# Optimization experiments

Measured on AMD Instinct MI355X. Metric: run time of the kernel, lower is better.

Reference implementation:

```python
import jax, jax.numpy as jnp
import numpy as np

B, S, D = 16, 38, 1792          # batch, seq_len, d_model = 768 + 2*512
H, DK = 4, 448                   # heads, head dim (D // H)
NP = 128                         # prototype rows before repeat
TOPK = 3                         # hard-coded in VqaPrototypeModel
INF = 768                        # qamodel.qa_outputs.in_features


def setup_inputs() -> dict:
    key = jax.random.key(0)
    ks = jax.random.split(key, 16)
    sc = lambda d: 1.0 / np.sqrt(d)
    inp = {
        "combined_features": jax.random.normal(ks[0], (B, S, D), jnp.float32),
        "prototype_vectors": jax.random.normal(ks[1], (1, NP, D), jnp.float32),
        "attention_mask": jnp.ones((B, S), jnp.int32),
        # MultiThreadMemory: 4 Linear(d_model, d_model) -> q, k, v, out
        "Wq": jax.random.normal(ks[2], (D, D), jnp.float32) * sc(D),
        "bq": jnp.zeros((D,), jnp.float32),
        "Wk": jax.random.normal(ks[3], (D, D), jnp.float32) * sc(D),
        "bk": jnp.zeros((D,), jnp.float32),
        "Wv": jax.random.normal(ks[4], (D, D), jnp.float32) * sc(D),
        "bv": jnp.zeros((D,), jnp.float32),
        "Wo": jax.random.normal(ks[5], (D, D), jnp.float32) * sc(D),
        "bo": jnp.zeros((D,), jnp.float32),
        # fc: Linear(2*d_model, in_features)
        "Wfc": jax.random.normal(ks[6], (2 * D, INF), jnp.float32) * sc(2 * D),
        "bfc": jnp.zeros((INF,), jnp.float32),
        # stub of qamodel.qa_outputs: Linear(in_features, 2)
        "Wqa": jax.random.normal(ks[7], (INF, 2), jnp.float32) * sc(INF),
        "bqa": jnp.zeros((2,), jnp.float32),
    }
    return inp


def reference(combined_features, prototype_vectors, attention_mask,
              Wq, bq, Wk, bk, Wv, bv, Wo, bo, Wfc, bfc, Wqa, bqa):
    b, s, d = combined_features.shape
    # prototype_vectors.repeat(batch_size, seq_length, 1) -> [B, S*NP, D]
    pv = jnp.tile(prototype_vectors, (b, s, 1))
    m = pv.shape[1]

    q = combined_features @ Wq + bq                     # [B,S,D]
    k = pv @ Wk + bk                                    # [B,M,D]
    v = pv @ Wv + bv                                    # [B,M,D]

    q = q.reshape(b, s, H, DK).transpose(0, 2, 1, 3)    # [B,H,S,DK]
    k = k.reshape(b, m, H, DK).transpose(0, 2, 1, 3)    # [B,H,M,DK]
    v = v.reshape(b, m, H, DK).transpose(0, 2, 1, 3)    # [B,H,M,DK]

    # memory_querying_responding: score + topk + gather + softmax + weighted sum
    scores = jnp.einsum('bhsd,bhmd->bhsm', q, k) / np.sqrt(DK)  # [B,H,S,M]
    sel_scores, idx = jax.lax.top_k(scores, TOPK)               # [B,H,S,TOPK]
    # gather selected prototype values: v[b,h,idx[b,h,s,:],:]
    sel_value = jnp.take_along_axis(v[:, :, None, :, :], idx[..., None], axis=3)
    # sel_value: [B,H,S,TOPK,DK]
    p_attn = jax.nn.softmax(sel_scores.astype(jnp.float32), axis=-1)
    x = jnp.einsum('bhsk,bhskd->bhsd', p_attn, sel_value)       # [B,H,S,DK]
    x = x.transpose(0, 2, 1, 3).reshape(b, s, H * DK)           # [B,S,D]
    response = x @ Wo + bo

    final = jnp.concatenate([combined_features, response], axis=2)  # [B,S,2D]
    reduced = final @ Wfc + bfc                                     # [B,S,INF]
    # qamodel stub: qa_outputs head -> start/end logits stacked on last dim
    logits = reduced @ Wqa + bqa                                    # [B,S,2]
    return logits
```

## Files before the change

### kernel.cpp

```cpp
#include <hip/hip_runtime.h>

#define TM 128
#define TN 128
#define BK 16
#define LDT 132

struct SP {
    const float *p0, *p1, *p2, *p3, *p4, *p5, *p6, *p7;
    float *q0, *q1, *q2;
};

__device__ __forceinline__ float wave_sum(float v) {
    #pragma unroll
    for (int off = 32; off; off >>= 1) v += __shfl_down(v, off);
    return v;
}

__device__ __forceinline__ void colvec2_unit(
    const float* __restrict__ A, int lda, const float* __restrict__ W,
    float* __restrict__ out, int K, int m, int lane)
{
    const float4* a = (const float4*)(A + (long)m * lda);
    float a0 = 0.f, a1 = 0.f;
    for (int i = 0; i < K / 256; ++i) {
        const int d4 = lane + 64 * i;
        float4 xv = a[d4];
        const float4* w = (const float4*)(W + (long)d4 * 8);
        float4 w0 = w[0], w1 = w[1];
        a0 += xv.x*w0.x + xv.y*w0.z + xv.z*w1.x + xv.w*w1.z;
        a1 += xv.x*w0.y + xv.y*w0.w + xv.z*w1.y + xv.w*w1.w;
    }
    a0 = wave_sum(a0); a1 = wave_sum(a1);
    if (lane == 0) { out[m * 2 + 0] = a0; out[m * 2 + 1] = a1; }
}

__device__ __forceinline__ void sbias_unit(
    const float* __restrict__ bq, const float* __restrict__ Kp,
    float* __restrict__ sb, int unit, int lane)
{
    const int h = unit >> 7, p = unit & 127;
    const float* kr = Kp + (long)p * 1792 + h * 448;
    const float* bh = bq + h * 448;
    float s = 0.f;
    #pragma unroll
    for (int i = 0; i < 7; ++i) s = fmaf(bh[lane + 64 * i], kr[lane + 64 * i], s);
    s = wave_sum(s);
    if (lane == 0) sb[unit] = s;
}

__device__ __forceinline__ void wvwoq_unit(
    const float* __restrict__ Wv, const float* __restrict__ WoQ,
    float* __restrict__ out, int d, int h, int lane)
{
    const float* wr = Wv + (long)d * 1792 + h * 448;
    const float* wq = WoQ + h * 448 * 2;
    float s0 = 0.f, s1 = 0.f;
    #pragma unroll
    for (int i = 0; i < 7; ++i) {
        const int j = lane + 64 * i;
        const float v = wr[j];
        s0 = fmaf(v, wq[j * 2 + 0], s0);
        s1 = fmaf(v, wq[j * 2 + 1], s1);
    }
    s0 = wave_sum(s0); s1 = wave_sum(s1);
    if (lane == 0) {
        out[((long)h * 1792 + d) * 2 + 0] = s0;
        out[((long)h * 1792 + d) * 2 + 1] = s1;
    }
}

__device__ __forceinline__ void bias_unit(
    const float* __restrict__ bv, const float* __restrict__ WoQ,
    const float* __restrict__ bfc, const float* __restrict__ Wqa,
    const float* __restrict__ bo, const float* __restrict__ WfbQ,
    const float* __restrict__ bqa,
    float* __restrict__ cv, float* __restrict__ const2, int unit, int lane)
{
    float s0 = 0.f, s1 = 0.f;
    if (unit < 4) {
        const int h = unit;
        #pragma unroll
        for (int i = 0; i < 7; ++i) {
            const int j = h * 448 + lane + 64 * i;
            const float v = bv[j];
            s0 = fmaf(v, WoQ[j * 2 + 0], s0);
            s1 = fmaf(v, WoQ[j * 2 + 1], s1);
        }
    } else {
        for (int k = lane; k < 1792; k += 64) {
            if (k < 768) {
                s0 = fmaf(bfc[k], Wqa[k * 2 + 0], s0);
                s1 = fmaf(bfc[k], Wqa[k * 2 + 1], s1);
            }
            s0 = fmaf(bo[k], WfbQ[k * 2 + 0], s0);
            s1 = fmaf(bo[k], WfbQ[k * 2 + 1], s1);
        }
    }
    s0 = wave_sum(s0); s1 = wave_sum(s1);
    if (lane == 0) {
        if (unit < 4) { cv[unit * 2 + 0] = s0; cv[unit * 2 + 1] = s1; }
        else          { const2[0] = s0 + bqa[0]; const2[1] = s1 + bqa[1]; }
    }
}

template<bool TRANSB, int SIDE>
__global__ __launch_bounds__(512) void gemm_f32(
    const float* __restrict__ A, int lda,
    const float* __restrict__ B, int ldb,
    float* __restrict__ C,
    int M, int N, int K,
    int nsplit, int nbb, int mainZ,
    long sAb, long sBb, SP sp)
{
    const int tid = threadIdx.x;
    if ((int)blockIdx.z >= mainZ) {
        const int bid = ((int)blockIdx.z - mainZ) * (gridDim.x * gridDim.y)
                      + blockIdx.y * gridDim.x + blockIdx.x;
        const int lane = tid & 63;
        const int u = bid * 8 + (tid >> 6);
        if constexpr (SIDE == 1) {
            if (u < 3584) colvec2_unit(sp.p0, 768, sp.p1, sp.q0, 768, u, lane);
        } else if constexpr (SIDE == 2) {
            if (u < 1792)       colvec2_unit(sp.p0, 1792, sp.p1, sp.q0, 1792, u, lane);
            else if (u < 2304)  sbias_unit(sp.p2, sp.p3, sp.q1, u - 1792, lane);
        } else if constexpr (SIDE == 3) {
            if (u < 7168)       wvwoq_unit(sp.p0, sp.p1, sp.q0, u % 1792, u / 1792, lane);
            else if (u < 7173)  bias_unit(sp.p2, sp.p1, sp.p3, sp.p4, sp.p5, sp.p6, sp.p7,
                                          sp.q1, sp.q2, u - 7168, lane);
        }
        return;
    }

    const int kb = blockIdx.z % nsplit;
    const int bb = blockIdx.z / nsplit;
    A += sAb * bb;
    B += sBb * bb;
    const int Kc = K / nsplit;
    const int kbeg = kb * Kc;

    __shared__ float As[2][BK][LDT];
    __shared__ float Bs[2][BK][LDT];

    const int tx = tid & 31, ty = tid >> 5;
    const int rowBase = blockIdx.y * TM;
    const int colBase = blockIdx.x * TN;

    const int ar  = tid >> 2;
    const int akq = (tid & 3) * 4;
    const int bkr = tid >> 5;
    const int bc4 = (tid & 31) * 4;
    const int bn  = tid >> 2;
    const int bkq = (tid & 3) * 4;

    const int row0 = rowBase + ar;
    const bool aok = row0 < M;

    float4 av, bv;
    auto loadA = [&](int k0) {
        av = make_float4(0.f, 0.f, 0.f, 0.f);
        if (aok) av = *(const float4*)&A[(long)row0 * lda + k0 + akq];
    };
    auto loadB = [&](int k0) {
        if (!TRANSB) bv = *(const float4*)&B[(long)(k0 + bkr) * ldb + colBase + bc4];
        else         bv = *(const float4*)&B[(long)(colBase + bn) * ldb + k0 + bkq];
    };
    auto stage = [&](int buf) {
        As[buf][akq + 0][ar] = av.x; As[buf][akq + 1][ar] = av.y;
        As[buf][akq + 2][ar] = av.z; As[buf][akq + 3][ar] = av.w;
        if (!TRANSB) {
            *(float4*)&Bs[buf][bkr][bc4] = bv;
        } else {
            Bs[buf][bkq + 0][bn] = bv.x; Bs[buf][bkq + 1][bn] = bv.y;
            Bs[buf][bkq + 2][bn] = bv.z; Bs[buf][bkq + 3][bn] = bv.w;
        }
    };

    float acc[8][4] = {};
    loadA(kbeg); loadB(kbeg);
    stage(0);
    __syncthreads();

    const int nk = Kc / BK;
    for (int t = 0; t < nk; ++t) {
        const int cur = t & 1;
        const bool more = (t + 1 < nk);
        if (more) { loadA(kbeg + (t + 1) * BK); loadB(kbeg + (t + 1) * BK); }
        #pragma unroll
        for (int kk = 0; kk < BK; ++kk) {
            float a[8], b[4];
            *(float4*)&a[0] = *(const float4*)&As[cur][kk][ty * 8];
            *(float4*)&a[4] = *(const float4*)&As[cur][kk][ty * 8 + 4];
            *(float4*)&b[0] = *(const float4*)&Bs[cur][kk][tx * 4];
            #pragma unroll
            for (int i = 0; i < 8; ++i)
                #pragma unroll
                for (int j = 0; j < 4; ++j)
                    acc[i][j] = fmaf(a[i], b[j], acc[i][j]);
        }
        if (more) stage(cur ^ 1);
        __syncthreads();
    }

    float* Cw = C + ((long)kb * nbb + bb) * (long)M * N;
    #pragma unroll
    for (int i = 0; i < 8; ++i) {
        const int row = rowBase + ty * 8 + i;
        if (row >= M) continue;
        *(float4*)&Cw[(long)row * N + colBase + tx * 4] =
            make_float4(acc[i][0], acc[i][1], acc[i][2], acc[i][3]);
    }
}

__global__ __launch_bounds__(256) void reduce_add(
    const float* __restrict__ part, float* __restrict__ out,
    const float* __restrict__ bias, int N, long sz, int nsplit)
{
    long i = (long)blockIdx.x * 256 + threadIdx.x;
    const long stride = (long)gridDim.x * 256;
    for (; i < sz; i += stride) {
        float s = 0.f;
        for (int z = 0; z < nsplit; ++z) s += part[z * sz + i];
        if (bias) s += bias[i % N];
        out[i] = s;
    }
}

__global__ __launch_bounds__(256) void argmax_lg_k(
    const float* __restrict__ Sp,
    const float* __restrict__ sbias,
    int* __restrict__ idx,
    const float* __restrict__ proto, const float* __restrict__ WvWoQ,
    const float* __restrict__ cv, float* __restrict__ LG)
{
    const int lane = threadIdx.x & 63;
    const int b = blockIdx.x;
    if (b < 608) {
        const int unit = b * 4 + (threadIdx.x >> 6);
        const int row = unit >> 2, h = unit & 3;
        float s0 = sbias[h * 128 + lane];
        float s1 = sbias[h * 128 + lane + 64];
        #pragma unroll
        for (int z = 0; z < 16; ++z) {
            const long base = ((long)(z * 4 + h) * 608 + row) * 128;
            s0 += Sp[base + lane];
            s1 += Sp[base + lane + 64];
        }
        float best = s0; int bi = lane;
        if (s1 > best) { best = s1; bi = lane + 64; }
        #pragma unroll
        for (int off = 32; off; off >>= 1) {
            float ov = __shfl_down(best, off);
            int   oi = __shfl_down(bi, off);
            if (ov > best || (ov == best && oi < bi)) { best = ov; bi = oi; }
        }
        if (lane == 0) idx[row * 4 + h] = bi;
    } else {
        const int unit = (b - 608) * 4 + (threadIdx.x >> 6);
        const int h = unit >> 7, p = unit & 127;
        const float4* a = (const float4*)(proto + (long)p * 1792);
        const float* W = WvWoQ + (long)h * 1792 * 2;
        float a0 = 0.f, a1 = 0.f;
        #pragma unroll
        for (int i = 0; i < 7; ++i) {
            const int d4 = lane + 64 * i;
            float4 xv = a[d4];
            const float4* w = (const float4*)(W + (long)d4 * 8);
            float4 w0 = w[0], w1 = w[1];
            a0 += xv.x*w0.x + xv.y*w0.z + xv.z*w1.x + xv.w*w1.z;
            a1 += xv.x*w0.y + xv.y*w0.w + xv.z*w1.y + xv.w*w1.w;
        }
        a0 = wave_sum(a0); a1 = wave_sum(a1);
        if (lane == 0) {
            LG[(h * 128 + p) * 2 + 0] = a0 + cv[h * 2 + 0];
            LG[(h * 128 + p) * 2 + 1] = a1 + cv[h * 2 + 1];
        }
    }
}

__global__ __launch_bounds__(256) void final_k(
    const float* __restrict__ X, const float* __restrict__ Wbig,
    const float* __restrict__ LG, const int* __restrict__ idx,
    const float* __restrict__ const2, float* __restrict__ out)
{
    const int lane = threadIdx.x & 63;
    const int row = blockIdx.x * 4 + (threadIdx.x >> 6);
    if (row >= 608) return;
    const float4* x = (const float4*)(X + (long)row * 1792);
    float a0 = 0.f, a1 = 0.f;
    #pragma unroll
    for (int i = 0; i < 7; ++i) {
        const int d4 = lane + 64 * i;
        float4 xv = x[d4];
        const float4* w = (const float4*)(Wbig + (long)d4 * 8);
        float4 w0 = w[0], w1 = w[1];
        a0 += xv.x*w0.x + xv.y*w0.z + xv.z*w1.x + xv.w*w1.z;
        a1 += xv.x*w0.y + xv.y*w0.w + xv.z*w1.y + xv.w*w1.w;
    }
    a0 = wave_sum(a0); a1 = wave_sum(a1);
    if (lane == 0) {
        float r0 = a0 + const2[0], r1 = a1 + const2[1];
        #pragma unroll
        for (int h = 0; h < 4; ++h) {
            const int p = idx[row * 4 + h];
            r0 += LG[(h * 128 + p) * 2 + 0];
            r1 += LG[(h * 128 + p) * 2 + 1];
        }
        out[row * 2 + 0] = r0;
        out[row * 2 + 1] = r1;
    }
}

extern "C" void kernel_launch(void* const* d_in, const int* in_sizes, int n_in,
                              void* d_out, int out_size, void* d_ws, size_t ws_size,
                              hipStream_t stream)
{
    const float* X     = (const float*)d_in[0];
    const float* proto = (const float*)d_in[1];
    const float* Wq  = (const float*)d_in[3];
    const float* bq  = (const float*)d_in[4];
    const float* Wk  = (const float*)d_in[5];
    const float* bk  = (const float*)d_in[6];
    const float* Wv  = (const float*)d_in[7];
    const float* bv  = (const float*)d_in[8];
    const float* Wo  = (const float*)d_in[9];
    const float* bo  = (const float*)d_in[10];
    const float* Wfc = (const float*)d_in[11];
    const float* bfc = (const float*)d_in[12];
    const float* Wqa = (const float*)d_in[13];
    const float* bqa = (const float*)d_in[14];
    float* out = (float*)d_out;

    float* ws = (float*)d_ws;
    float* P      = ws;
    float* Kp     = P + 4980736;
    float* W2b    = Kp + 229376;
    float* sbias  = W2b + 917504;
    float* WbigB  = sbias + 512;
    float* WoQ    = WbigB + 7168;
    float* WvWoQ  = WoQ + 3584;
    float* LG     = WvWoQ + 14336;
    float* cv     = LG + 1024;
    float* const2 = cv + 8;
    int*   idx    = (int*)(const2 + 8);
    float* WfbQ   = WbigB + 1792 * 2;

    dim3 gblk(512), blk(256);

    {
        SP sp{}; sp.p0 = Wfc; sp.p1 = Wqa; sp.q0 = WbigB;
        gemm_f32<false, 1><<<dim3(14, 1, 14 + 32), gblk, 0, stream>>>(
            proto, 1792, Wk, 1792, P, 128, 1792, 1792, 14, 1, 14, 0, 0, sp);
    }
    reduce_add<<<dim3(896), blk, 0, stream>>>(P, Kp, bk, 1792, 229376L, 14);

    {
        SP sp{}; sp.p0 = Wo; sp.p1 = WfbQ; sp.q0 = WoQ; sp.p2 = bq; sp.p3 = Kp; sp.q1 = sbias;
        gemm_f32<true, 2><<<dim3(1, 14, 16 + 21), gblk, 0, stream>>>(
            Wq, 1792, Kp, 1792, P, 1792, 128, 448, 4, 4, 16, 448, 448, sp);
    }
    reduce_add<<<dim3(1792), blk, 0, stream>>>(P, W2b, nullptr, 1, 917504L, 4);

    {
        SP sp{}; sp.p0 = Wv; sp.p1 = WoQ; sp.q0 = WvWoQ;
        sp.p2 = bv; sp.p3 = bfc; sp.p4 = Wqa; sp.p5 = bo; sp.p6 = WfbQ; sp.p7 = bqa;
        sp.q1 = cv; sp.q2 = const2;
        gemm_f32<false, 3><<<dim3(1, 5, 64 + 180), gblk, 0, stream>>>(
            X, 1792, W2b, 128, P, 608, 128, 1792, 16, 4, 64, 0, 229376L, sp);
    }
    argmax_lg_k<<<dim3(736), blk, 0, stream>>>(P, sbias, idx, proto, WvWoQ, cv, LG);

    final_k<<<dim3(152), blk, 0, stream>>>(X, WbigB, LG, idx, const2, out);
}
```

Before: 99.56 us.

## Fuse argmax with final projection and raise split-K factors in GEMMs

Merges the argmax kernel and the final logits kernel into one. Each wave now picks the top prototype per head and computes its logit contribution directly as a dot product of the prototype row with WvWoQ, so the separate LG table precompute and the idx round trip through global memory are gone. The split-K counts of all three GEMMs are raised (14→28, 4→7, 16→28) to launch more blocks, and the workspace offsets grow to hold the extra partials. In exchange the fused kernel recomputes four prototype dot products per row, and the larger splits add more partial sums to write and reduce.

After: 122.1 us. 1.23x slower.

```diff
diff --git a/kernel.cpp b/kernel.cpp
--- a/kernel.cpp
+++ b/kernel.cpp
@@ -225,22 +225,26 @@
     }
 }
 
-__global__ __launch_bounds__(256) void argmax_lg_k(
+__global__ __launch_bounds__(256) void argmax_final_k(
     const float* __restrict__ Sp,
     const float* __restrict__ sbias,
-    int* __restrict__ idx,
-    const float* __restrict__ proto, const float* __restrict__ WvWoQ,
-    const float* __restrict__ cv, float* __restrict__ LG)
+    const float* __restrict__ X, const float* __restrict__ Wbig,
+    const float* __restrict__ WvWoQ,
+    const float* __restrict__ proto,
+    const float* __restrict__ cv, const float* __restrict__ const2,
+    float* __restrict__ out)
 {
     const int lane = threadIdx.x & 63;
-    const int b = blockIdx.x;
-    if (b < 608) {
-        const int unit = b * 4 + (threadIdx.x >> 6);
-        const int row = unit >> 2, h = unit & 3;
+    const int row = blockIdx.x * 4 + (threadIdx.x >> 6);
+    if (row >= 608) return;
+
+    int sel[4];
+    #pragma unroll
+    for (int h = 0; h < 4; ++h) {
         float s0 = sbias[h * 128 + lane];
         float s1 = sbias[h * 128 + lane + 64];
-        #pragma unroll
-        for (int z = 0; z < 16; ++z) {
+        #pragma unroll 4
+        for (int z = 0; z < 28; ++z) {
             const long base = ((long)(z * 4 + h) * 608 + row) * 128;
             s0 += Sp[base + lane];
             s1 += Sp[base + lane + 64];
@@ -253,60 +257,31 @@
             int   oi = __shfl_down(bi, off);
             if (ov > best || (ov == best && oi < bi)) { best = ov; bi = oi; }
         }
-        if (lane == 0) idx[row * 4 + h] = bi;
-    } else {
-        const int unit = (b - 608) * 4 + (threadIdx.x >> 6);
-        const int h = unit >> 7, p = unit & 127;
-        const float4* a = (const float4*)(proto + (long)p * 1792);
-        const float* W = WvWoQ + (long)h * 1792 * 2;
-        float a0 = 0.f, a1 = 0.f;
+        sel[h] = __shfl(bi, 0);
+    }
+
+    float a0 = 0.f, a1 = 0.f;
+    auto dot2 = [&](const float* a, const float* w) {
+        const float4* av = (const float4*)a;
         #pragma unroll
         for (int i = 0; i < 7; ++i) {
             const int d4 = lane + 64 * i;
-            float4 xv = a[d4];
-            const float4* w = (const float4*)(W + (long)d4 * 8);
-            float4 w0 = w[0], w1 = w[1];
+            float4 xv = av[d4];
+            const float4* wp = (const float4*)(w + (long)d4 * 8);
+            float4 w0 = wp[0], w1 = wp[1];
             a0 += xv.x*w0.x + xv.y*w0.z + xv.z*w1.x + xv.w*w1.z;
             a1 += xv.x*w0.y + xv.y*w0.w + xv.z*w1.y + xv.w*w1.w;
         }
-        a0 = wave_sum(a0); a1 = wave_sum(a1);
-        if (lane == 0) {
-            LG[(h * 128 + p) * 2 + 0] = a0 + cv[h * 2 + 0];
-            LG[(h * 128 + p) * 2 + 1] = a1 + cv[h * 2 + 1];
-        }
-    }
-}
-
-__global__ __launch_bounds__(256) void final_k(
-    const float* __restrict__ X, const float* __restrict__ Wbig,
-    const float* __restrict__ LG, const int* __restrict__ idx,
-    const float* __restrict__ const2, float* __restrict__ out)
-{
-    const int lane = threadIdx.x & 63;
-    const int row = blockIdx.x * 4 + (threadIdx.x >> 6);
-    if (row >= 608) return;
-    const float4* x = (const float4*)(X + (long)row * 1792);
-    float a0 = 0.f, a1 = 0.f;
-    #pragma unroll
-    for (int i = 0; i < 7; ++i) {
-        const int d4 = lane + 64 * i;
-        float4 xv = x[d4];
-        const float4* w = (const float4*)(Wbig + (long)d4 * 8);
-        float4 w0 = w[0], w1 = w[1];
-        a0 += xv.x*w0.x + xv.y*w0.z + xv.z*w1.x + xv.w*w1.z;
-        a1 += xv.x*w0.y + xv.y*w0.w + xv.z*w1.y + xv.w*w1.w;
-    }
+    };
+    dot2(X + (long)row * 1792, Wbig);
+    #pragma unroll
+    for (int h = 0; h < 4; ++h)
+        dot2(proto + (long)sel[h] * 1792, WvWoQ + (long)h * 3584);
+
     a0 = wave_sum(a0); a1 = wave_sum(a1);
     if (lane == 0) {
-        float r0 = a0 + const2[0], r1 = a1 + const2[1];
-        #pragma unroll
-        for (int h = 0; h < 4; ++h) {
-            const int p = idx[row * 4 + h];
-            r0 += LG[(h * 128 + p) * 2 + 0];
-            r1 += LG[(h * 128 + p) * 2 + 1];
-        }
-        out[row * 2 + 0] = r0;
-        out[row * 2 + 1] = r1;
+        out[row * 2 + 0] = a0 + const2[0] + cv[0] + cv[2] + cv[4] + cv[6];
+        out[row * 2 + 1] = a1 + const2[1] + cv[1] + cv[3] + cv[5] + cv[7];
     }
 }
 
@@ -332,42 +307,39 @@
 
     float* ws = (float*)d_ws;
     float* P      = ws;
-    float* Kp     = P + 4980736;
+    float* Kp     = P + 8716288;
     float* W2b    = Kp + 229376;
     float* sbias  = W2b + 917504;
     float* WbigB  = sbias + 512;
     float* WoQ    = WbigB + 7168;
     float* WvWoQ  = WoQ + 3584;
-    float* LG     = WvWoQ + 14336;
-    float* cv     = LG + 1024;
+    float* cv     = WvWoQ + 14336;
     float* const2 = cv + 8;
-    int*   idx    = (int*)(const2 + 8);
-    float* WfbQ   = WbigB + 1792 * 2;
+    float* WfbQ   = WbigB + 3584;
 
     dim3 gblk(512), blk(256);
 
     {
         SP sp{}; sp.p0 = Wfc; sp.p1 = Wqa; sp.q0 = WbigB;
-        gemm_f32<false, 1><<<dim3(14, 1, 14 + 32), gblk, 0, stream>>>(
-            proto, 1792, Wk, 1792, P, 128, 1792, 1792, 14, 1, 14, 0, 0, sp);
-    }
-    reduce_add<<<dim3(896), blk, 0, stream>>>(P, Kp, bk, 1792, 229376L, 14);
+        gemm_f32<false, 1><<<dim3(14, 1, 28 + 32), gblk, 0, stream>>>(
+            proto, 1792, Wk, 1792, P, 128, 1792, 1792, 28, 1, 28, 0, 0, sp);
+    }
+    reduce_add<<<dim3(896), blk, 0, stream>>>(P, Kp, bk, 1792, 229376L, 28);
 
     {
         SP sp{}; sp.p0 = Wo; sp.p1 = WfbQ; sp.q0 = WoQ; sp.p2 = bq; sp.p3 = Kp; sp.q1 = sbias;
-        gemm_f32<true, 2><<<dim3(1, 14, 16 + 21), gblk, 0, stream>>>(
-            Wq, 1792, Kp, 1792, P, 1792, 128, 448, 4, 4, 16, 448, 448, sp);
-    }
-    reduce_add<<<dim3(1792), blk, 0, stream>>>(P, W2b, nullptr, 1, 917504L, 4);
+        gemm_f32<true, 2><<<dim3(1, 14, 28 + 21), gblk, 0, stream>>>(
+            Wq, 1792, Kp, 1792, P, 1792, 128, 448, 7, 4, 28, 448, 448, sp);
+    }
+    reduce_add<<<dim3(1792), blk, 0, stream>>>(P, W2b, nullptr, 1, 917504L, 7);
 
     {
         SP sp{}; sp.p0 = Wv; sp.p1 = WoQ; sp.q0 = WvWoQ;
         sp.p2 = bv; sp.p3 = bfc; sp.p4 = Wqa; sp.p5 = bo; sp.p6 = WfbQ; sp.p7 = bqa;
         sp.q1 = cv; sp.q2 = const2;
-        gemm_f32<false, 3><<<dim3(1, 5, 64 + 180), gblk, 0, stream>>>(
-            X, 1792, W2b, 128, P, 608, 128, 1792, 16, 4, 64, 0, 229376L, sp);
-    }
-    argmax_lg_k<<<dim3(736), blk, 0, stream>>>(P, sbias, idx, proto, WvWoQ, cv, LG);
-
-    final_k<<<dim3(152), blk, 0, stream>>>(X, WbigB, LG, idx, const2, out);
-}
+        gemm_f32<false, 3><<<dim3(1, 5, 112 + 180), gblk, 0, stream>>>(
+            X, 1792, W2b, 128, P, 608, 128, 1792, 28, 4, 112, 0, 229376L, sp);
+    }
+    argmax_final_k<<<dim3(152), blk, 0, stream>>>(
+        P, sbias, X, WbigB, WvWoQ, proto, cv, const2, out);
+}
```
